# Optimization experiments

Hardware: AMD Instinct MI355X
Metric: run time of the kernel (lower is better)

The kernel has to match this reference:

```python
import jax, jax.numpy as jnp
import numpy as np

KS = 3          # kernel_size
PAD = 1         # padding
G = 4           # num_groups
C_IN = 64
C_OUT = 64
K = KS * KS     # 9 sampling points
EPS = 1e-5


def bilinear_sample(img, py, px):
    """img: [B,Cg,H,W]; py,px: [B,K,H,W] -> [B,Cg,K,H,W] (zero outside)."""
    B, Cg, H, W = img.shape
    y0 = jnp.floor(py); x0 = jnp.floor(px)
    wy1 = py - y0; wx1 = px - x0
    wy0 = 1.0 - wy1; wx0 = 1.0 - wx1
    img_flat = img.reshape(B, Cg, H * W)

    def gather(yc, xc):
        valid = (yc >= 0) & (yc <= H - 1) & (xc >= 0) & (xc <= W - 1)
        yi = jnp.clip(yc, 0, H - 1).astype(jnp.int32)
        xi = jnp.clip(xc, 0, W - 1).astype(jnp.int32)
        flat = (yi * W + xi).reshape(B, 1, K * H * W)
        v = jnp.take_along_axis(img_flat, flat, axis=2).reshape(B, Cg, K, H, W)
        return v * valid[:, None].astype(img.dtype)

    v00 = gather(y0, x0)
    v01 = gather(y0, x0 + 1.0)
    v10 = gather(y0 + 1.0, x0)
    v11 = gather(y0 + 1.0, x0 + 1.0)
    return (v00 * (wy0 * wx0)[:, None] + v01 * (wy0 * wx1)[:, None]
            + v10 * (wy1 * wx0)[:, None] + v11 * (wy1 * wx1)[:, None])


def deform_conv_group(x_g, offset, mask, w, b):
    """torchvision-style modulated deform_conv2d, stride=1, dilation=1.
    x_g: [B,Ci,H,W]; offset: [B,2K,H,W] (y,x interleaved); mask: [B,K,H,W];
    w: [Co,Ci,KS,KS]; b: [Co]."""
    B, Ci, H, W = x_g.shape
    Co = w.shape[0]
    ky = (jnp.arange(K) // KS).astype(x_g.dtype)
    kx = (jnp.arange(K) % KS).astype(x_g.dtype)
    hh = jnp.arange(H, dtype=x_g.dtype)
    ww = jnp.arange(W, dtype=x_g.dtype)
    off_y = offset[:, 0::2]  # [B,K,H,W]
    off_x = offset[:, 1::2]
    py = hh[None, None, :, None] - PAD + ky[None, :, None, None] + off_y
    px = ww[None, None, None, :] - PAD + kx[None, :, None, None] + off_x
    val = bilinear_sample(x_g, py, px) * mask[:, None]  # [B,Ci,K,H,W]
    out = jnp.einsum('bckhw,ock->bohw', val, w.reshape(Co, Ci, K))
    return out + b[None, :, None, None]


def setup_inputs() -> dict:
    key = jax.random.key(0)
    ks = jax.random.split(key, 8)
    B, H, W = 4, 128, 128
    Cg_in = C_IN // G
    Cg_out = C_OUT // G
    inp = {
        'x': jax.random.normal(ks[0], (B, C_IN, H, W), dtype=jnp.float32),
        'w_om': jax.random.normal(ks[1], (G * 3 * K, C_IN), dtype=jnp.float32) * 0.02,
        'b_om': jnp.zeros((G * 3 * K,), dtype=jnp.float32),
        'dcn_w': jax.random.normal(ks[2], (G, Cg_out, Cg_in, KS, KS), dtype=jnp.float32) * 0.1,
        'dcn_b': jnp.zeros((G, Cg_out), dtype=jnp.float32),
        'gn_w': jnp.ones((C_OUT,), dtype=jnp.float32),
        'gn_b': jnp.zeros((C_OUT,), dtype=jnp.float32),
        'offset_scale': jnp.ones((1,), dtype=jnp.float32),
    }
    return inp


def reference(x, w_om, b_om, dcn_w, dcn_b, gn_w, gn_b, offset_scale):
    B, C, H, W = x.shape
    ch_per_group = C // G
    # 1x1 offset/mask conv
    om = jnp.einsum('bchw,oc->bohw', x, w_om) + b_om[None, :, None, None]
    outs = []
    for g in range(G):
        x_g = x[:, g * ch_per_group:(g + 1) * ch_per_group]
        s = g * 3 * K
        offset_g = om[:, s:s + 2 * K] * offset_scale[0]
        mask_g = jax.nn.sigmoid(om[:, s + 2 * K:s + 3 * K])
        outs.append(deform_conv_group(x_g, offset_g, mask_g, dcn_w[g], dcn_b[g]))
    out = jnp.concatenate(outs, axis=1)  # [B,C_OUT,H,W]
    # GroupNorm(G, C_OUT)
    og = out.reshape(B, G, C_OUT // G, H, W)
    mu = jnp.mean(og, axis=(2, 3, 4), keepdims=True)
    var = jnp.var(og, axis=(2, 3, 4), keepdims=True)
    og = (og - mu) * jax.lax.rsqrt(var + EPS)
    out = og.reshape(B, C_OUT, H, W) * gn_w[None, :, None, None] + gn_b[None, :, None, None]
    return jax.nn.gelu(out, approximate=False)
```

## Files before the change

### kernel.cpp

```cpp
#include <hip/hip_runtime.h>
#include <math.h>

#define GRP   4
#define K     9
#define PAD   1
#define C_IN  64
#define CG    16
#define HH    128
#define WW    128
#define BB    4
#define HW    (HH*WW)

typedef __attribute__((ext_vector_type(8))) _Float16 f16x8;
typedef __attribute__((ext_vector_type(2))) _Float16 f16x2;
typedef __attribute__((ext_vector_type(4))) float    f32x4;

union F16Frag { f16x8 f; _Float16 h[8]; f16x2 p[4]; uint w[4]; uint4 q; };
union YX      { uint u; f16x2 h2; };

#define XT_OFF     0
#define XT_BYTES   ((size_t)16 * HW * 16 * 2)
#define OM_OFF     XT_BYTES
#define OM_BYTES   ((size_t)16 * HW * 28 * 2)
#define FR1_OFF    (OM_OFF + OM_BYTES)
#define FR1_BYTES  (14 * 64 * 16)
#define FR2_OFF    (FR1_OFF + FR1_BYTES)
#define FR2_BYTES  (20 * 64 * 16)
#define PART_OFF   (FR2_OFF + FR2_BYTES)
#define PART_BYTES (2048 * 2 * 4)
#define STATS_OFF  (PART_OFF + PART_BYTES)
#define NEED_BYTES (STATS_OFF + 128)
#define FB_PART_OFF  XT_BYTES
#define FB_STATS_OFF (XT_BYTES + 1024 * 2 * 4)

__global__ __launch_bounds__(256) void make_frags(const float* __restrict__ w_om,
                                                  const float* __restrict__ dcn_w,
                                                  uint4* __restrict__ frags1,
                                                  uint4* __restrict__ frags2)
{
    const int t    = blockIdx.x * 256 + threadIdx.x;
    const int lane = t & 63;
    const int lr   = lane & 15, lj = lane >> 4;
    const int f    = t >> 6;
    F16Frag r;
    #pragma unroll
    for (int e = 0; e < 4; ++e) r.w[e] = 0u;
    if (f < 14) {
        const int nt = f >> 1, s = f & 1;
        const int col = nt * 16 + lr;
        const int g = col / 28, oo = col - 28 * g;
        if (oo < 27) {
            const float* src = w_om + (size_t)(g * 27 + oo) * C_IN + s * 32 + lj * 8;
            #pragma unroll
            for (int e = 0; e < 8; ++e) r.h[e] = (_Float16)src[e];
        }
        frags1[f * 64 + lane] = r.q;
    } else if (f < 34) {
        const int f2 = f - 14;
        const int g = f2 / 5, s = f2 - 5 * g;
        const int kp = 2 * s + (lj >> 1);
        const int cib = (lj & 1) * 8;
        if (kp < 9) {
            #pragma unroll
            for (int e = 0; e < 8; ++e)
                r.h[e] = (_Float16)dcn_w[((size_t)(g * CG + lr) * CG + cib + e) * 9 + kp];
        }
        frags2[f2 * 64 + lane] = r.q;
    }
}

__global__ __launch_bounds__(256, 4) void om_gemm_t(
    const float* __restrict__ x,
    const uint4* __restrict__ frags1,
    const float* __restrict__ b_om,
    const float* __restrict__ offset_scale,
    _Float16* __restrict__ xt4,
    _Float16* __restrict__ om16)
{
    const int tid  = threadIdx.x;
    const int wave = tid >> 6, lane = tid & 63;
    const int lr   = lane & 15, lj = lane >> 4;
    const int bpix0   = blockIdx.x * 64 + wave * 16;
    const int pixflat = bpix0 + lr;
    const int b       = pixflat >> 14;
    const int pixb    = pixflat & (HW - 1);
    const float scale = offset_scale[0];

    const float* xs = x + (size_t)b * C_IN * HW + pixb;
    F16Frag A0, A1;
    #pragma unroll
    for (int e = 0; e < 8; ++e) A0.h[e] = (_Float16)xs[(size_t)(lj * 8 + e) * HW];
    #pragma unroll
    for (int e = 0; e < 8; ++e) A1.h[e] = (_Float16)xs[(size_t)(32 + lj * 8 + e) * HW];

    const int g0 = (lj >> 1), g1 = 2 + (lj >> 1);
    const int hf = (lj & 1) * 8;
    *(uint4*)(xt4 + ((size_t)(b * 4 + g0) * HW + pixb) * 16 + hf) = A0.q;
    *(uint4*)(xt4 + ((size_t)(b * 4 + g1) * HW + pixb) * 16 + hf) = A1.q;

    int g_[7], oo_[7];
    float bo_[7];
    #pragma unroll
    for (int nt = 0; nt < 7; ++nt) {
        const int col = nt * 16 + lr;
        const int g = col / 28, oo = col - 28 * g;
        g_[nt] = g; oo_[nt] = oo;
        bo_[nt] = (oo < 27) ? b_om[g * 27 + oo] : 0.0f;
    }

    const int bq = bpix0 >> 14;
    const int pq = bpix0 & (HW - 1);
    #pragma unroll
    for (int nt = 0; nt < 7; ++nt) {
        F16Frag B0, B1;
        B0.q = frags1[(nt * 2 + 0) * 64 + lane];
        B1.q = frags1[(nt * 2 + 1) * 64 + lane];
        f32x4 C = {0, 0, 0, 0};
        C = __builtin_amdgcn_mfma_f32_16x16x32_f16(A0.f, B0.f, C, 0, 0, 0);
        C = __builtin_amdgcn_mfma_f32_16x16x32_f16(A1.f, B1.f, C, 0, 0, 0);
        const int g = g_[nt], oo = oo_[nt];
        if (oo < 27) {
            const size_t base = ((size_t)(bq * 4 + g) * HW + pq + lj * 4);
            #pragma unroll
            for (int r = 0; r < 4; ++r) {
                float v = C[r] + bo_[nt];
                v = (oo < 18) ? v * scale : 1.0f / (1.0f + __expf(-v));
                om16[(base + r) * 28 + oo] = (_Float16)v;
            }
        }
    }
}

__global__ __launch_bounds__(256, 4) void dcn_sample(
    const _Float16* __restrict__ xt4,
    const _Float16* __restrict__ om16,
    const uint4* __restrict__ frags2,
    const float* __restrict__ dcn_b,
    float* __restrict__ out,
    float* __restrict__ partials)
{
    const int tid = threadIdx.x;
    const int blk = blockIdx.x;
    const int xcd = blk & 7;
    const int q   = blk >> 3;
    const int bg  = xcd * 2 + (q >> 7);
    const int row = q & 127;
    const int b   = bg >> 2, g = bg & 3;
    const int wave = tid >> 6, lane = tid & 63;
    const int lr = lane & 15;
    const int lj = lane >> 4;

    __shared__ float red[512];

    F16Frag B2[5];
    #pragma unroll
    for (int s = 0; s < 5; ++s) B2[s].q = frags2[(g * 5 + s) * 64 + lane];
    const float cbias = dcn_b[g * CG + lr];

    const _Float16* xg = xt4 + (size_t)bg * HW * 16 + (lj & 1) * 8;
    const uint* omw = (const uint*)om16;

    const int pbase = (bg << 14) + row * WW + wave * 32 + lr;
    uint     yxv[2][5];
    _Float16 mv [2][5];
    #pragma unroll
    for (int t = 0; t < 2; ++t) {
        const int p = pbase + t * 16;
        #pragma unroll
        for (int s = 0; s < 5; ++s) {
            const int kp = 2 * s + (lj >> 1);
            const int kc = (kp < 9) ? kp : 8;
            yxv[t][s] = omw[(size_t)p * 14 + kc];
            mv [t][s] = om16[(size_t)p * 28 + 18 + kc];
        }
    }

    float gs = 0.0f, gss = 0.0f;

    #pragma unroll
    for (int t = 0; t < 2; ++t) {
        const int col0 = wave * 32 + t * 16;
        const int pix0 = row * WW + col0;

        f32x4 C2 = {cbias, cbias, cbias, cbias};
        #pragma unroll
        for (int s = 0; s < 5; ++s) {
            const int  kp  = 2 * s + (lj >> 1);
            const bool kok = (kp < 9);
            const int  kc  = kok ? kp : 8;

            YX yx; yx.u = yxv[t][s];
            const float offy = (float)yx.h2[0];
            const float offx = (float)yx.h2[1];
            const float m    = kok ? (float)mv[t][s] : 0.0f;

            const float py = (float)(row       - PAD + kc / 3) + offy;
            const float px = (float)(col0 + lr - PAD + kc % 3) + offx;

            const float y0f = floorf(py), x0f = floorf(px);
            const int   y0  = (int)y0f,   x0  = (int)x0f;
            const float wy1 = py - y0f,   wx1 = px - x0f;
            const float wy0 = 1.0f - wy1, wx0 = 1.0f - wx1;
            const bool vy0 = (y0 >= 0)  & (y0 <  HH);
            const bool vy1 = (y0 >= -1) & (y0 <  HH - 1);
            const bool vx0 = (x0 >= 0)  & (x0 <  WW);
            const bool vx1 = (x0 >= -1) & (x0 <  WW - 1);
            const int yi0 = min(max(y0,     0), HH - 1);
            const int yi1 = min(max(y0 + 1, 0), HH - 1);
            const int xi0 = min(max(x0,     0), WW - 1);
            const int xi1 = min(max(x0 + 1, 0), WW - 1);
            const float my0 = wy0 * m, my1 = wy1 * m;
            const float w00 = (vy0 & vx0) ? my0 * wx0 : 0.0f;
            const float w01 = (vy0 & vx1) ? my0 * wx1 : 0.0f;
            const float w10 = (vy1 & vx0) ? my1 * wx0 : 0.0f;
            const float w11 = (vy1 & vx1) ? my1 * wx1 : 0.0f;

            F16Frag t00, t01, t10, t11;
            t00.q = *(const uint4*)(xg + (size_t)(yi0 * WW + xi0) * 16);
            t01.q = *(const uint4*)(xg + (size_t)(yi0 * WW + xi1) * 16);
            t10.q = *(const uint4*)(xg + (size_t)(yi1 * WW + xi0) * 16);
            t11.q = *(const uint4*)(xg + (size_t)(yi1 * WW + xi1) * 16);

            const _Float16 h00 = (_Float16)w00, h01 = (_Float16)w01;
            const _Float16 h10 = (_Float16)w10, h11 = (_Float16)w11;
            const f16x2 W00 = {h00, h00}, W01 = {h01, h01};
            const f16x2 W10 = {h10, h10}, W11 = {h11, h11};

            F16Frag A;
            #pragma unroll
            for (int d = 0; d < 4; ++d) {
                f16x2 acc = t00.p[d] * W00;
                acc += t01.p[d] * W01;
                acc += t10.p[d] * W10;
                acc += t11.p[d] * W11;
                A.p[d] = acc;
            }
            C2 = __builtin_amdgcn_mfma_f32_16x16x32_f16(A.f, B2[s].f, C2, 0, 0, 0);
        }

        float4 st;
        #pragma unroll
        for (int r = 0; r < 4; ++r) {
            const float v = C2[r];
            gs += v; gss += v * v;
            (&st.x)[r] = v;
        }
        *(float4*)(out + ((size_t)b * 64 + g * CG + lr) * HW + pix0 + lj * 4) = st;
    }

    red[tid] = gs; red[256 + tid] = gss;
    __syncthreads();
    for (int st2 = 128; st2 > 0; st2 >>= 1) {
        if (tid < st2) {
            red[tid]       += red[tid + st2];
            red[256 + tid] += red[256 + tid + st2];
        }
        __syncthreads();
    }
    if (tid == 0) {
        partials[(bg * 128 + row) * 2]     = red[0];
        partials[(bg * 128 + row) * 2 + 1] = red[256];
    }
}

__global__ __launch_bounds__(256) void gn_gelu2(float* __restrict__ out,
                                                const float* __restrict__ partials,
                                                const float* __restrict__ gn_w,
                                                const float* __restrict__ gn_b)
{
    const int blk = blockIdx.x;
    const int tid = threadIdx.x;
    const int bc  = blk >> 4;
    const int c   = bc & 63;
    const int bg  = ((bc >> 6) << 2) + (c >> 4);

    __shared__ float ls[256];
    ls[tid] = partials[bg * 256 + tid];
    __syncthreads();
    #pragma unroll
    for (int st = 128; st >= 2; st >>= 1) {
        if (tid < st) ls[tid] += ls[tid + st];
        __syncthreads();
    }
    const float n  = (float)(CG * HW);
    const float mu = ls[0] / n;
    const float rs = rsqrtf(ls[1] / n - mu * mu + 1e-5f);
    const float sw = gn_w[c] * rs;
    const float sb = gn_b[c] - mu * sw;

    const int idx = blk * 256 + tid;
    float4 v = ((const float4*)out)[idx];
    float rr[4] = {v.x, v.y, v.z, v.w};
    #pragma unroll
    for (int jj = 0; jj < 4; ++jj) {
        const float t = rr[jj] * sw + sb;
        rr[jj] = t * 0.5f * (1.0f + erff(t * 0.70710678118654752f));
    }
    ((float4*)out)[idx] = make_float4(rr[0], rr[1], rr[2], rr[3]);
}


__global__ __launch_bounds__(256) void transpose_pack(const float* __restrict__ x,
                                                      _Float16* __restrict__ xt)
{
    const int t   = blockIdx.x * 256 + threadIdx.x;
    const int qq  = t & 3;
    const int p2  = t >> 2;
    const int pix = p2 & (HW - 1);
    const int b   = p2 >> 14;
    const float* xs = x + ((size_t)b * C_IN + qq * 16) * HW + pix;
    F16Frag f0, f1;
    #pragma unroll
    for (int j = 0; j < 8; ++j) f0.h[j] = (_Float16)xs[(size_t)j * HW];
    #pragma unroll
    for (int j = 0; j < 8; ++j) f1.h[j] = (_Float16)xs[(size_t)(8 + j) * HW];
    uint4* dst = (uint4*)(xt + ((size_t)b * HW + pix) * 64 + qq * 16);
    dst[0] = f0.q;
    dst[1] = f1.q;
}

__global__ __launch_bounds__(256, 4) void dcn_fused_fb(
    const _Float16* __restrict__ xt,
    const float* __restrict__ w_om,
    const float* __restrict__ b_om,
    const float* __restrict__ dcn_w,
    const float* __restrict__ dcn_b,
    const float* __restrict__ offset_scale,
    float* __restrict__ out,
    float* __restrict__ partials)
{
    const int tid = threadIdx.x;
    const int blk = blockIdx.x;
    const int xcd = blk & 7;
    const int q   = blk >> 3;
    const int bg  = xcd * 2 + (q >> 6);
    const int tb  = q & 63;
    const int b   = bg >> 2, g = bg & 3;
    const int wave = tid >> 6, lane = tid & 63;
    const int lr = lane & 15, lj = lane >> 4;

    __shared__ float om_lds[4][16][33];
    __shared__ float red[512];

    F16Frag B1[2][2];
    #pragma unroll
    for (int s = 0; s < 2; ++s)
    #pragma unroll
    for (int nt = 0; nt < 2; ++nt) {
        const int o = nt * 16 + lr;
        if (o < 27) {
            const float* src = w_om + (size_t)(g * 27 + o) * C_IN + s * 32 + lj * 8;
            #pragma unroll
            for (int e = 0; e < 8; ++e) B1[s][nt].h[e] = (_Float16)src[e];
        } else {
            #pragma unroll
            for (int e = 0; e < 4; ++e) B1[s][nt].w[e] = 0u;
        }
    }
    F16Frag B2[5];
    #pragma unroll
    for (int s = 0; s < 5; ++s) {
        const int kp  = 2 * s + (lj >> 1);
        const int cib = (lj & 1) * 8;
        if (kp < 9) {
            const float* src = dcn_w + ((size_t)(g * CG + lr) * CG + cib) * 9 + kp;
            #pragma unroll
            for (int e = 0; e < 8; ++e) B2[s].h[e] = (_Float16)src[(size_t)e * 9];
        } else {
            #pragma unroll
            for (int e = 0; e < 4; ++e) B2[s].w[e] = 0u;
        }
    }

    const float scale = offset_scale[0];
    const float bo0   = b_om[g * 27 + lr];
    const float bo1   = (lr < 11) ? b_om[g * 27 + 16 + lr] : 0.0f;
    const float cbias = dcn_b[g * CG + lr];

    const _Float16* xtb = xt + (size_t)b * HW * 64;
    const _Float16* xg  = xtb + g * CG + (lj & 1) * 8;
    float gs = 0.0f, gss = 0.0f;

    for (int t = 0; t < 4; ++t) {
        const int pix0 = tb * 256 + wave * 64 + t * 16;
        const int row  = pix0 >> 7;
        const int col0 = pix0 & 127;

        f32x4 C0 = {0, 0, 0, 0}, C1 = {0, 0, 0, 0};
        #pragma unroll
        for (int s = 0; s < 2; ++s) {
            F16Frag A;
            A.q = *(const uint4*)(xtb + (size_t)(pix0 + lr) * 64 + s * 32 + lj * 8);
            C0 = __builtin_amdgcn_mfma_f32_16x16x32_f16(A.f, B1[s][0].f, C0, 0, 0, 0);
            C1 = __builtin_amdgcn_mfma_f32_16x16x32_f16(A.f, B1[s][1].f, C1, 0, 0, 0);
        }
        #pragma unroll
        for (int r = 0; r < 4; ++r) {
            const int prow = lj * 4 + r;
            om_lds[wave][prow][lr] = (C0[r] + bo0) * scale;
            const float v1 = C1[r] + bo1;
            const int o1 = 16 + lr;
            om_lds[wave][prow][o1] = (o1 < 18) ? v1 * scale
                                   : 1.0f / (1.0f + __expf(-v1));
        }

        f32x4 C2 = {cbias, cbias, cbias, cbias};
        #pragma unroll
        for (int s = 0; s < 5; ++s) {
            const int  kp  = 2 * s + (lj >> 1);
            const bool kok = (kp < 9);
            const int  kc  = kok ? kp : 8;
            const float offy = om_lds[wave][lr][2 * kc];
            const float offx = om_lds[wave][lr][2 * kc + 1];
            const float m    = kok ? om_lds[wave][lr][18 + kc] : 0.0f;
            const float py = (float)(row  - PAD + kc / 3) + offy;
            const float px = (float)(col0 + lr - PAD + kc % 3) + offx;

            const float y0f = floorf(py), x0f = floorf(px);
            const int   y0  = (int)y0f,   x0  = (int)x0f;
            const float wy1 = py - y0f,   wx1 = px - x0f;
            const float wy0 = 1.0f - wy1, wx0 = 1.0f - wx1;
            const bool vy0 = (y0 >= 0)  & (y0 <  HH);
            const bool vy1 = (y0 >= -1) & (y0 <  HH - 1);
            const bool vx0 = (x0 >= 0)  & (x0 <  WW);
            const bool vx1 = (x0 >= -1) & (x0 <  WW - 1);
            const int yi0 = min(max(y0,     0), HH - 1);
            const int yi1 = min(max(y0 + 1, 0), HH - 1);
            const int xi0 = min(max(x0,     0), WW - 1);
            const int xi1 = min(max(x0 + 1, 0), WW - 1);
            const float my0 = wy0 * m, my1 = wy1 * m;
            const float w00 = (vy0 & vx0) ? my0 * wx0 : 0.0f;
            const float w01 = (vy0 & vx1) ? my0 * wx1 : 0.0f;
            const float w10 = (vy1 & vx0) ? my1 * wx0 : 0.0f;
            const float w11 = (vy1 & vx1) ? my1 * wx1 : 0.0f;

            F16Frag t00, t01, t10, t11;
            t00.q = *(const uint4*)(xg + (size_t)(yi0 * WW + xi0) * 64);
            t01.q = *(const uint4*)(xg + (size_t)(yi0 * WW + xi1) * 64);
            t10.q = *(const uint4*)(xg + (size_t)(yi1 * WW + xi0) * 64);
            t11.q = *(const uint4*)(xg + (size_t)(yi1 * WW + xi1) * 64);

            const _Float16 h00 = (_Float16)w00, h01 = (_Float16)w01;
            const _Float16 h10 = (_Float16)w10, h11 = (_Float16)w11;
            const f16x2 W00 = {h00, h00}, W01 = {h01, h01};
            const f16x2 W10 = {h10, h10}, W11 = {h11, h11};

            F16Frag A;
            #pragma unroll
            for (int d = 0; d < 4; ++d) {
                f16x2 acc = t00.p[d] * W00;
                acc += t01.p[d] * W01;
                acc += t10.p[d] * W10;
                acc += t11.p[d] * W11;
                A.p[d] = acc;
            }
            C2 = __builtin_amdgcn_mfma_f32_16x16x32_f16(A.f, B2[s].f, C2, 0, 0, 0);
        }

        float4 st;
        #pragma unroll
        for (int r = 0; r < 4; ++r) {
            const float v = C2[r];
            gs += v; gss += v * v;
            (&st.x)[r] = v;
        }
        *(float4*)(out + ((size_t)b * 64 + g * CG + lr) * HW + pix0 + lj * 4) = st;
    }

    red[tid] = gs; red[256 + tid] = gss;
    __syncthreads();
    for (int st2 = 128; st2 > 0; st2 >>= 1) {
        if (tid < st2) {
            red[tid]       += red[tid + st2];
            red[256 + tid] += red[256 + tid + st2];
        }
        __syncthreads();
    }
    if (tid == 0) {
        partials[(bg * 64 + tb) * 2]     = red[0];
        partials[(bg * 64 + tb) * 2 + 1] = red[256];
    }
}

__global__ __launch_bounds__(64) void gn_finalize(const float* __restrict__ partials,
                                                  float* __restrict__ stats,
                                                  int per_bg)
{
    const int bg = blockIdx.x;
    const int t  = threadIdx.x;
    float s = 0.0f, ss = 0.0f;
    for (int i = t; i < per_bg; i += 64) {
        s  += partials[(bg * per_bg + i) * 2];
        ss += partials[(bg * per_bg + i) * 2 + 1];
    }
    #pragma unroll
    for (int off = 32; off > 0; off >>= 1) {
        s  += __shfl_down(s, off);
        ss += __shfl_down(ss, off);
    }
    if (t == 0) {
        const float n   = (float)(CG * HW);
        const float mu  = s / n;
        const float var = ss / n - mu * mu;
        stats[bg * 2]     = mu;
        stats[bg * 2 + 1] = rsqrtf(var + 1e-5f);
    }
}

__global__ __launch_bounds__(256) void gn_gelu(float* __restrict__ out,
                                               const float* __restrict__ stats,
                                               const float* __restrict__ gn_w,
                                               const float* __restrict__ gn_b)
{
    const int idx = blockIdx.x * 256 + threadIdx.x;
    const int bc  = idx >> 12;
    const int c   = bc & 63;
    const int bg  = ((bc >> 6) << 2) + (c >> 4);

    const float mu = stats[bg * 2];
    const float rs = stats[bg * 2 + 1];
    const float sw = gn_w[c] * rs;
    const float sb = gn_b[c] - mu * sw;

    float4 v = ((const float4*)out)[idx];
    float rr[4] = {v.x, v.y, v.z, v.w};
    #pragma unroll
    for (int jj = 0; jj < 4; ++jj) {
        const float t = rr[jj] * sw + sb;
        rr[jj] = t * 0.5f * (1.0f + erff(t * 0.70710678118654752f));
    }
    ((float4*)out)[idx] = make_float4(rr[0], rr[1], rr[2], rr[3]);
}


extern "C" void kernel_launch(void* const* d_in, const int* in_sizes, int n_in,
                              void* d_out, int out_size, void* d_ws, size_t ws_size,
                              hipStream_t stream) {
    const float* x            = (const float*)d_in[0];
    const float* w_om         = (const float*)d_in[1];
    const float* b_om         = (const float*)d_in[2];
    const float* dcn_w        = (const float*)d_in[3];
    const float* dcn_b        = (const float*)d_in[4];
    const float* gn_w         = (const float*)d_in[5];
    const float* gn_b         = (const float*)d_in[6];
    const float* offset_scale = (const float*)d_in[7];
    float* out = (float*)d_out;
    char*  ws  = (char*)d_ws;

    _Float16* xt = (_Float16*)(ws + XT_OFF);

    if (ws_size >= NEED_BYTES) {
        _Float16* om16   = (_Float16*)(ws + OM_OFF);
        uint4* frags1    = (uint4*)(ws + FR1_OFF);
        uint4* frags2    = (uint4*)(ws + FR2_OFF);
        float* partials  = (float*)(ws + PART_OFF);

        make_frags<<<9, 256, 0, stream>>>(w_om, dcn_w, frags1, frags2);
        om_gemm_t<<<1024, 256, 0, stream>>>(x, frags1, b_om, offset_scale, xt, om16);
        dcn_sample<<<2048, 256, 0, stream>>>(xt, om16, frags2, dcn_b, out, partials);
        gn_gelu2<<<4096, 256, 0, stream>>>(out, partials, gn_w, gn_b);
    } else {
        float* partials = (float*)(ws + FB_PART_OFF);
        float* stats    = (float*)(ws + FB_STATS_OFF);
        transpose_pack<<<1024, 256, 0, stream>>>(x, xt);
        dcn_fused_fb<<<1024, 256, 0, stream>>>(xt, w_om, b_om, dcn_w, dcn_b,
                                               offset_scale, out, partials);
        gn_finalize<<<16, 64, 0, stream>>>(partials, stats, 64);
        gn_gelu<<<(BB * 64 * HW / 4) / 256, 256, 0, stream>>>(out, stats, gn_w, gn_b);
    }
}
```

Before: 60.31 us.

## Stage six-row input window in LDS and store offsets/masks as per-k planes

The sampling kernel now copies a six-row window of the transposed fp16 input around the current output row into shared memory. Bilinear taps are read from LDS, with a fallback to global memory when a sample falls outside the window. Separately, the offset/mask tensor is split into per-tap planes (packed y/x pairs and masks) so the sampler's loads become coalesced along pixels. This adds 24KB of LDS per block and a barrier, which may lower occupancy, and adds a divergent fallback path for large offsets.

Result: faster. 54.93 us (-8.9%).

```diff
diff --git a/kernel.cpp b/kernel.cpp
--- a/kernel.cpp
+++ b/kernel.cpp
@@ -18,18 +18,20 @@
 union F16Frag { f16x8 f; _Float16 h[8]; f16x2 p[4]; uint w[4]; uint4 q; };
 union YX      { uint u; f16x2 h2; };
 
+#define PLANE      ((size_t)16 * HW)
 #define XT_OFF     0
 #define XT_BYTES   ((size_t)16 * HW * 16 * 2)
-#define OM_OFF     XT_BYTES
-#define OM_BYTES   ((size_t)16 * HW * 28 * 2)
-#define FR1_OFF    (OM_OFF + OM_BYTES)
+#define OMYX_OFF   XT_BYTES
+#define OMYX_BYTES (9 * PLANE * 4)
+#define OMM_OFF    (OMYX_OFF + OMYX_BYTES)
+#define OMM_BYTES  (9 * PLANE * 2)
+#define FR1_OFF    (OMM_OFF + OMM_BYTES)
 #define FR1_BYTES  (14 * 64 * 16)
 #define FR2_OFF    (FR1_OFF + FR1_BYTES)
 #define FR2_BYTES  (20 * 64 * 16)
 #define PART_OFF   (FR2_OFF + FR2_BYTES)
 #define PART_BYTES (2048 * 2 * 4)
-#define STATS_OFF  (PART_OFF + PART_BYTES)
-#define NEED_BYTES (STATS_OFF + 128)
+#define NEED_BYTES (PART_OFF + PART_BYTES + 128)
 #define FB_PART_OFF  XT_BYTES
 #define FB_STATS_OFF (XT_BYTES + 1024 * 2 * 4)
 
@@ -75,7 +77,8 @@
     const float* __restrict__ b_om,
     const float* __restrict__ offset_scale,
     _Float16* __restrict__ xt4,
-    _Float16* __restrict__ om16)
+    _Float16* __restrict__ om_yx,
+    _Float16* __restrict__ om_m)
 {
     const int tid  = threadIdx.x;
     const int wave = tid >> 6, lane = tid & 63;
@@ -121,11 +124,18 @@
         const int g = g_[nt], oo = oo_[nt];
         if (oo < 27) {
             const size_t base = ((size_t)(bq * 4 + g) * HW + pq + lj * 4);
-            #pragma unroll
-            for (int r = 0; r < 4; ++r) {
-                float v = C[r] + bo_[nt];
-                v = (oo < 18) ? v * scale : 1.0f / (1.0f + __expf(-v));
-                om16[(base + r) * 28 + oo] = (_Float16)v;
+            if (oo < 18) {
+                const int k = oo >> 1, comp = oo & 1;
+                #pragma unroll
+                for (int r = 0; r < 4; ++r)
+                    om_yx[((size_t)k * PLANE + base + r) * 2 + comp] =
+                        (_Float16)((C[r] + bo_[nt]) * scale);
+            } else {
+                const int k = oo - 18;
+                #pragma unroll
+                for (int r = 0; r < 4; ++r)
+                    om_m[(size_t)k * PLANE + base + r] =
+                        (_Float16)(1.0f / (1.0f + __expf(-(C[r] + bo_[nt]))));
             }
         }
     }
@@ -133,7 +143,8 @@
 
 __global__ __launch_bounds__(256, 4) void dcn_sample(
     const _Float16* __restrict__ xt4,
-    const _Float16* __restrict__ om16,
+    const uint* __restrict__ om_yx_u,
+    const _Float16* __restrict__ om_m,
     const uint4* __restrict__ frags2,
     const float* __restrict__ dcn_b,
     float* __restrict__ out,
@@ -149,16 +160,25 @@
     const int wave = tid >> 6, lane = tid & 63;
     const int lr = lane & 15;
     const int lj = lane >> 4;
-
+    const int hsel = lj & 1;
+
+    __shared__ uint4 sm4[1536];
     __shared__ float red[512];
+
+    const int wr0 = min(max(row - 2, 0), HH - 6);
+    {
+        const uint4* src = (const uint4*)(xt4 + ((size_t)bg * HW + wr0 * WW) * 16);
+        #pragma unroll
+        for (int i = tid; i < 1536; i += 256) {
+            const int dst = ((i >> 8) * 2 + (i & 1)) * 128 + ((i >> 1) & 127);
+            sm4[dst] = src[i];
+        }
+    }
 
     F16Frag B2[5];
     #pragma unroll
     for (int s = 0; s < 5; ++s) B2[s].q = frags2[(g * 5 + s) * 64 + lane];
     const float cbias = dcn_b[g * CG + lr];
-
-    const _Float16* xg = xt4 + (size_t)bg * HW * 16 + (lj & 1) * 8;
-    const uint* omw = (const uint*)om16;
 
     const int pbase = (bg << 14) + row * WW + wave * 32 + lr;
     uint     yxv[2][5];
@@ -170,10 +190,14 @@
         for (int s = 0; s < 5; ++s) {
             const int kp = 2 * s + (lj >> 1);
             const int kc = (kp < 9) ? kp : 8;
-            yxv[t][s] = omw[(size_t)p * 14 + kc];
-            mv [t][s] = om16[(size_t)p * 28 + 18 + kc];
-        }
-    }
+            yxv[t][s] = om_yx_u[(size_t)kc * PLANE + p];
+            mv [t][s] = om_m  [(size_t)kc * PLANE + p];
+        }
+    }
+
+    __syncthreads();
+    const _Float16* smh = (const _Float16*)sm4;
+    const _Float16* xgf = xt4 + (size_t)bg * HW * 16 + hsel * 8;
 
     float gs = 0.0f, gss = 0.0f;
 
@@ -215,11 +239,24 @@
             const float w10 = (vy1 & vx0) ? my1 * wx0 : 0.0f;
             const float w11 = (vy1 & vx1) ? my1 * wx1 : 0.0f;
 
+            const int ly0 = yi0 - wr0, ly1 = yi1 - wr0;
+            const bool okw = (ly0 >= 0) & (ly1 <= 5);
+            const int cy0 = min(max(ly0, 0), 5);
+            const int cy1 = min(max(ly1, 0), 5);
+            const int r0 = (cy0 * 2 + hsel) * 128;
+            const int r1 = (cy1 * 2 + hsel) * 128;
+
             F16Frag t00, t01, t10, t11;
-            t00.q = *(const uint4*)(xg + (size_t)(yi0 * WW + xi0) * 16);
-            t01.q = *(const uint4*)(xg + (size_t)(yi0 * WW + xi1) * 16);
-            t10.q = *(const uint4*)(xg + (size_t)(yi1 * WW + xi0) * 16);
-            t11.q = *(const uint4*)(xg + (size_t)(yi1 * WW + xi1) * 16);
+            t00.q = *(const uint4*)(smh + (size_t)(r0 + xi0) * 8);
+            t01.q = *(const uint4*)(smh + (size_t)(r0 + xi1) * 8);
+            t10.q = *(const uint4*)(smh + (size_t)(r1 + xi0) * 8);
+            t11.q = *(const uint4*)(smh + (size_t)(r1 + xi1) * 8);
+            if (!okw) {
+                t00.q = *(const uint4*)(xgf + (size_t)(yi0 * WW + xi0) * 16);
+                t01.q = *(const uint4*)(xgf + (size_t)(yi0 * WW + xi1) * 16);
+                t10.q = *(const uint4*)(xgf + (size_t)(yi1 * WW + xi0) * 16);
+                t11.q = *(const uint4*)(xgf + (size_t)(yi1 * WW + xi1) * 16);
+            }
 
             const _Float16 h00 = (_Float16)w00, h01 = (_Float16)w01;
             const _Float16 h10 = (_Float16)w10, h11 = (_Float16)w11;
@@ -550,14 +587,17 @@
     _Float16* xt = (_Float16*)(ws + XT_OFF);
 
     if (ws_size >= NEED_BYTES) {
-        _Float16* om16   = (_Float16*)(ws + OM_OFF);
+        _Float16* om_yx  = (_Float16*)(ws + OMYX_OFF);
+        _Float16* om_m   = (_Float16*)(ws + OMM_OFF);
         uint4* frags1    = (uint4*)(ws + FR1_OFF);
         uint4* frags2    = (uint4*)(ws + FR2_OFF);
         float* partials  = (float*)(ws + PART_OFF);
 
         make_frags<<<9, 256, 0, stream>>>(w_om, dcn_w, frags1, frags2);
-        om_gemm_t<<<1024, 256, 0, stream>>>(x, frags1, b_om, offset_scale, xt, om16);
-        dcn_sample<<<2048, 256, 0, stream>>>(xt, om16, frags2, dcn_b, out, partials);
+        om_gemm_t<<<1024, 256, 0, stream>>>(x, frags1, b_om, offset_scale,
+                                            xt, om_yx, om_m);
+        dcn_sample<<<2048, 256, 0, stream>>>(xt, (const uint*)om_yx, om_m,
+                                             frags2, dcn_b, out, partials);
         gn_gelu2<<<4096, 256, 0, stream>>>(out, partials, gn_w, gn_b);
     } else {
         float* partials = (float*)(ws + FB_PART_OFF);
```
